# Optimization experiments

Hardware: AMD Instinct MI355X
Metric: run time of the kernel (lower is better)

The kernel has to match this reference:

```python
import jax, jax.numpy as jnp
import numpy as np
import math

B, T, C, NH = 4, 2048, 1024, 16
D = C // NH  # 64, rotary_dim == D

def _rope_tables():
    inv_freq = 1.0 / (10000.0 ** (np.arange(0, D, 2, dtype=np.float32) / D))
    t = np.arange(T, dtype=np.float32)
    freqs = np.outer(t, inv_freq)                 # [T, D/2]
    emb = np.concatenate([freqs, freqs], axis=-1)  # [T, D]
    return jnp.asarray(np.cos(emb))[None], jnp.asarray(np.sin(emb))[None]  # [1,T,D]

def setup_inputs() -> dict:
    key = jax.random.key(0)
    ks = jax.random.split(key, 3)
    x = jax.random.normal(ks[0], (B, T, C), dtype=jnp.float32)
    w_attn = jax.random.normal(ks[1], (3 * C, C), dtype=jnp.float32) * (1.0 / math.sqrt(C))
    b_attn = jnp.zeros((3 * C,), dtype=jnp.float32)
    w_proj = jax.random.normal(ks[2], (C, C), dtype=jnp.float32) * (1.0 / math.sqrt(C))
    b_proj = jnp.zeros((C,), dtype=jnp.float32)
    cos, sin = _rope_tables()
    return {"x": x, "w_attn": w_attn, "b_attn": b_attn,
            "w_proj": w_proj, "b_proj": b_proj, "cos": cos, "sin": sin}

def _rotate_half(u):
    u1, u2 = jnp.split(u, 2, axis=-1)
    return jnp.concatenate([-u2, u1], axis=-1)

def reference(x, w_attn, b_attn, w_proj, b_proj, cos, sin):
    Bx, Tx, Cx = x.shape
    nh, d = NH, Cx // NH
    # fused QKV projection (torch Linear: y = x @ W^T + b)
    qkv = x @ w_attn.T + b_attn                      # [B,T,3C]
    q, k, v = jnp.split(qkv, 3, axis=-1)
    q = q.reshape(Bx, Tx, nh, d).transpose(0, 2, 1, 3)  # [B,nh,T,d]
    k = k.reshape(Bx, Tx, nh, d).transpose(0, 2, 1, 3)
    v = v.reshape(Bx, Tx, nh, d).transpose(0, 2, 1, 3)
    # RoPE (rotary_dim == d, full head)
    c = cos[:, None, :, :]  # [1,1,T,d]
    s = sin[:, None, :, :]
    q = q * c + _rotate_half(q) * s
    k = k * c + _rotate_half(k) * s
    # naive causal attention
    scores = jnp.einsum("bhqd,bhkd->bhqk", q, k) / math.sqrt(d)
    causal = jnp.tril(jnp.ones((Tx, Tx), dtype=bool))
    scores = jnp.where(causal[None, None], scores, -jnp.inf)
    att = jax.nn.softmax(scores, axis=-1)
    y = jnp.einsum("bhqk,bhkd->bhqd", att, v)        # [B,nh,T,d]
    y = y.transpose(0, 2, 1, 3).reshape(Bx, Tx, Cx)
    return y @ w_proj.T + b_proj
```

## Files before the change

kernel.cpp:

```cpp
#include <hip/hip_runtime.h>

typedef __bf16 bf16_t;
typedef bf16_t bf16x8 __attribute__((ext_vector_type(8)));
typedef bf16_t bf16x4 __attribute__((ext_vector_type(4)));
typedef float f32x4 __attribute__((ext_vector_type(4)));

constexpr int BATCH = 4, SEQ = 2048, CH = 1024, NHEAD = 16, HD = 64;
constexpr int BM = 128, BN = 128, BKK = 64;

#define LGKM_FENCE() __asm__ __volatile__("s_waitcnt lgkmcnt(0)" ::: "memory")
#define VM_FENCE() __asm__ __volatile__("s_waitcnt vmcnt(0)" ::: "memory")

__device__ __forceinline__ void g2lds16(const bf16_t* g, bf16_t* l) {
  __builtin_amdgcn_global_load_lds((__attribute__((address_space(1))) void*)(g),
                                   (__attribute__((address_space(3))) void*)(l),
                                   16, 0, 0);
}

__device__ __forceinline__ f32x4 mfma16(bf16x8 a, bf16x8 b, f32x4 c) {
  return __builtin_amdgcn_mfma_f32_16x16x32_bf16(a, b, c, 0, 0, 0);
}

__global__ __launch_bounds__(256) void cvt3_kernel(const float4* __restrict__ x,
                                                   ushort4* __restrict__ dx,
                                                   const float4* __restrict__ wa,
                                                   ushort4* __restrict__ dwa,
                                                   const float4* __restrict__ wp,
                                                   ushort4* __restrict__ dwp) {
  int bid = blockIdx.x;
  const float4* s;
  ushort4* d;
  int i;
  if (bid < 8192) {
    s = x; d = dx; i = bid * 256 + threadIdx.x;
  } else if (bid < 11264) {
    s = wa; d = dwa; i = (bid - 8192) * 256 + threadIdx.x;
  } else {
    s = wp; d = dwp; i = (bid - 11264) * 256 + threadIdx.x;
  }
  float4 f = s[i];
  ushort4 o;
  o.x = __builtin_bit_cast(unsigned short, (bf16_t)f.x);
  o.y = __builtin_bit_cast(unsigned short, (bf16_t)f.y);
  o.z = __builtin_bit_cast(unsigned short, (bf16_t)f.z);
  o.w = __builtin_bit_cast(unsigned short, (bf16_t)f.w);
  d[i] = o;
}

__device__ __forceinline__ void gemm_mainloop(const bf16_t* __restrict__ A,
                                              const bf16_t* __restrict__ W, int Kdim,
                                              int m0, int n0,
                                              bf16_t* As, bf16_t* Bs,
                                              f32x4 acc[4][4]) {
  const int tid = threadIdx.x;
  const int lane = tid & 63;
  const int w = tid >> 6;
  const int quad = lane >> 4, l16 = lane & 15;
  const int wm = (w >> 1) << 6, wn = (w & 1) << 6;
  const int srow = tid >> 3;
  const int scol = ((tid & 7) ^ (srow & 7)) << 3;
  const int dcol = (tid & 7) << 3;
  const int key = l16 & 15 & 7;
  const bf16_t* ga[4];
  const bf16_t* gb[4];
  bf16_t *la[4], *lb[4];
#pragma unroll
  for (int p = 0; p < 4; p++) {
    int row = p * 32 + srow;
    ga[p] = A + (size_t)(m0 + row) * Kdim + scol;
    gb[p] = W + (size_t)(n0 + row) * Kdim + scol;
    la[p] = As + row * BKK + dcol;
    lb[p] = Bs + row * BKK + dcol;
  }
  for (int k0 = 0; k0 < Kdim; k0 += BKK) {
#pragma unroll
    for (int p = 0; p < 4; p++) g2lds16(ga[p] + k0, la[p]);
#pragma unroll
    for (int p = 0; p < 4; p++) g2lds16(gb[p] + k0, lb[p]);
    VM_FENCE();
    __syncthreads();
#pragma unroll
    for (int ki = 0; ki < 2; ki++) {
      bf16x8 av[4], bv[4];
#pragma unroll
      for (int i = 0; i < 4; i++)
        av[i] = *(const bf16x8*)&As[(wm + i * 16 + l16) * BKK +
                                    ((((ki << 2) | quad) ^ key) << 3)];
#pragma unroll
      for (int i = 0; i < 4; i++)
        bv[i] = *(const bf16x8*)&Bs[(wn + i * 16 + l16) * BKK +
                                    ((((ki << 2) | quad) ^ key) << 3)];
#pragma unroll
      for (int mi = 0; mi < 4; mi++)
#pragma unroll
        for (int ni = 0; ni < 4; ni++)
          acc[mi][ni] = mfma16(av[mi], bv[ni], acc[mi][ni]);
    }
    __syncthreads();
  }
}

constexpr float SCL = 0.125f * 1.44269504089f;

__global__ __launch_bounds__(256) void qkv_rope_kernel(
    const bf16_t* __restrict__ X, const bf16_t* __restrict__ Wa,
    const float* __restrict__ ba, const float* __restrict__ cosT,
    const float* __restrict__ sinT, bf16_t* __restrict__ Q,
    bf16_t* __restrict__ Ko, bf16_t* __restrict__ VT) {
  constexpr int TSTRIDE = 68;
  __shared__ __align__(16) char smem[4 * 64 * TSTRIDE * 2];
  bf16_t* As = (bf16_t*)smem;
  bf16_t* Bs = As + BM * BKK;

  f32x4 acc[4][4];
#pragma unroll
  for (int i = 0; i < 4; i++)
#pragma unroll
    for (int j = 0; j < 4; j++) acc[i][j] = (f32x4){0.f, 0.f, 0.f, 0.f};

  const int id = blockIdx.x;
  const int sid = ((id & 7) * 192) + (id >> 3);
  const int n0 = (sid % 24) * BN;
  const int m0 = (sid / 24) * BM;
  gemm_mainloop(X, Wa, CH, m0, n0, As, Bs, acc);

  const int tid = threadIdx.x, lane = tid & 63, w = tid >> 6;
  const int quad = lane >> 4, l16 = lane & 15;
  const int wm = (w >> 1) << 6, wn = (w & 1) << 6;
  const int nbase = n0 + wn;
  const int part = nbase >> 10;
  const int h = (nbase & 1023) >> 6;
  const int mbase = m0 + wm;
  const int bb = mbase >> 11;
  const size_t headbase = ((size_t)(bb * NHEAD + h)) * SEQ * HD;

  if (part < 2) {
    bf16_t* O = (part == 0) ? Q : Ko;
    const float post = (part == 0) ? SCL : 1.0f;
#pragma unroll
    for (int mi = 0; mi < 4; mi++)
#pragma unroll
      for (int r = 0; r < 4; r++) {
        int m = mbase + mi * 16 + quad * 4 + r;
        int t = m & (SEQ - 1);
        const float* cr = cosT + t * HD;
        const float* sr = sinT + t * HD;
        size_t rowo = headbase + (size_t)t * HD;
#pragma unroll
        for (int ni = 0; ni < 2; ni++) {
          int d0 = ni * 16 + l16, d1 = d0 + 32;
          float v0 = acc[mi][ni][r] + ba[nbase + d0];
          float v1 = acc[mi][ni + 2][r] + ba[nbase + d1];
          float r0 = (v0 * cr[d0] - v1 * sr[d0]) * post;
          float r1 = (v1 * cr[d1] + v0 * sr[d1]) * post;
          O[rowo + d0] = (bf16_t)r0;
          O[rowo + d1] = (bf16_t)r1;
        }
      }
  } else {
    bf16_t* tb = (bf16_t*)smem + w * 64 * TSTRIDE;
    int t0 = mbase & (SEQ - 1);
#pragma unroll
    for (int mi = 0; mi < 4; mi++)
#pragma unroll
      for (int ni = 0; ni < 4; ni++) {
        int d = ni * 16 + l16;
        float bias = ba[nbase + d];
#pragma unroll
        for (int r = 0; r < 4; r++) {
          float v = acc[mi][ni][r] + bias;
          tb[d * TSTRIDE + mi * 16 + quad * 4 + r] = (bf16_t)v;
        }
      }
    LGKM_FENCE();
    int half = lane >> 5, l5 = lane & 31;
    size_t vbase = ((size_t)(bb * NHEAD + h)) * HD * SEQ;
#pragma unroll
    for (int it = 0; it < 32; it++) {
      int d = it * 2 + half;
      unsigned int val = *(const unsigned int*)&tb[d * TSTRIDE + l5 * 2];
      *(unsigned int*)&VT[vbase + (size_t)d * SEQ + t0 + l5 * 2] = val;
    }
  }
}

__device__ __forceinline__ void sm_update(f32x4 (&s)[4], float& lr,
                                          bf16_t* Prow, int quad,
                                          int swz, bool domask, int lim) {
  if (domask) {
#pragma unroll
    for (int ni = 0; ni < 4; ni++)
#pragma unroll
      for (int r = 0; r < 4; r++)
        if (ni * 16 + r > lim) s[ni][r] = -1e30f;
  }
  float sum = 0.f;
#pragma unroll
  for (int ni = 0; ni < 4; ni++) {
    float p0 = __builtin_exp2f(s[ni][0]);
    float p1 = __builtin_exp2f(s[ni][1]);
    float p2 = __builtin_exp2f(s[ni][2]);
    float p3 = __builtin_exp2f(s[ni][3]);
    bf16x4 pk = {(bf16_t)p0, (bf16_t)p1, (bf16_t)p2, (bf16_t)p3};
    *(bf16x4*)&Prow[(((ni << 2) | quad) ^ (swz << 1)) << 2] = pk;
    sum += (p0 + p1) + (p2 + p3);
  }
  lr += sum;
}

__global__ __launch_bounds__(256) void flash_kernel(const bf16_t* __restrict__ Q,
                                                    const bf16_t* __restrict__ Kg,
                                                    const bf16_t* __restrict__ VT,
                                                    bf16_t* __restrict__ att) {
  __shared__ __align__(16) bf16_t Ks[2][64 * 64];
  __shared__ __align__(16) bf16_t Vs[2][64 * 64];
  __shared__ __align__(16) bf16_t Pt[4][16 * 64];
  const int tid = threadIdx.x, w = tid >> 6, lane = tid & 63;
  const int quad = lane >> 4, l16 = lane & 15;
  const int p = (int)blockIdx.x >> 6;
  const int bh = (int)blockIdx.x & 63;
  const bf16_t* Qp = Q + (size_t)bh * SEQ * HD;
  const bf16_t* Kb = Kg + (size_t)bh * SEQ * HD;
  const bf16_t* Vb = VT + (size_t)bh * HD * SEQ;
  const int grow = lane >> 3;
  const int gj8 = ((lane & 7) ^ grow) * 8;
  const int i0 = w * 2;
  const int sw = l16 & 7;
  const int swz = l16 >> 1;
  const int bloc = bh >> 4, hh = bh & 15;
  bf16_t* Pw = &Pt[w][l16 * 64];
  const int rs0 = (quad ^ swz) << 3;
  const int rs1 = ((4 + quad) ^ swz) << 3;

  auto stage = [&](int kcs, int b) {
#pragma unroll
    for (int ii = 0; ii < 2; ii++) {
      int i = i0 + ii;
      g2lds16(Kb + (size_t)(kcs + i * 8 + grow) * HD + gj8, &Ks[b][(i * 64 + lane) * 8]);
      g2lds16(Vb + (size_t)(i * 8 + grow) * SEQ + kcs + gj8, &Vs[b][(i * 64 + lane) * 8]);
    }
  };

  for (int sp = 0; sp < 2; ++sp) {
    const int j = sp ? p : 31 - p;
    const int m = j * 64 + w * 16;
    const int nch = j + 1;
    bf16x8 aq0 = *(const bf16x8*)&Qp[(size_t)(m + l16) * HD + quad * 8];
    bf16x8 aq1 = *(const bf16x8*)&Qp[(size_t)(m + l16) * HD + 32 + quad * 8];
    float lr = 0.f;
    f32x4 y[4];
#pragma unroll
    for (int ni = 0; ni < 4; ni++) y[ni] = (f32x4){0.f, 0.f, 0.f, 0.f};

    stage(0, 0);
    VM_FENCE();
    __syncthreads();

    for (int c = 0; c < nch; ++c) {
      const int kc = c * 64, buf = c & 1;
      if (c + 1 < nch) stage(kc + 64, buf ^ 1);
      f32x4 s[4];
#pragma unroll
      for (int ni = 0; ni < 4; ni++) {
        bf16x8 k0 = *(const bf16x8*)&Ks[buf][((ni * 16 + l16) * 8 + (quad ^ sw)) * 8];
        bf16x8 k1 = *(const bf16x8*)&Ks[buf][((ni * 16 + l16) * 8 + ((4 + quad) ^ sw)) * 8];
        f32x4 z = (f32x4){0.f, 0.f, 0.f, 0.f};
        s[ni] = mfma16(k1, aq1, mfma16(k0, aq0, z));
      }
      sm_update(s, lr, Pw, quad, swz, c == nch - 1, m + l16 - kc - quad * 4);
      LGKM_FENCE();
      bf16x8 p0 = *(const bf16x8*)&Pw[rs0];
      bf16x8 p1 = *(const bf16x8*)&Pw[rs1];
#pragma unroll
      for (int ni = 0; ni < 4; ni++) {
        bf16x8 v0 = *(const bf16x8*)&Vs[buf][((ni * 16 + l16) * 8 + (quad ^ sw)) * 8];
        bf16x8 v1 = *(const bf16x8*)&Vs[buf][((ni * 16 + l16) * 8 + ((4 + quad) ^ sw)) * 8];
        y[ni] = mfma16(v1, p1, mfma16(v0, p0, y[ni]));
      }
      VM_FENCE();
      __syncthreads();
    }

    lr += __shfl_xor(lr, 16);
    lr += __shfl_xor(lr, 32);
    float inv = 1.f / lr;
    size_t rb = ((size_t)bloc * SEQ + m + l16) * CH + hh * HD + quad * 4;
#pragma unroll
    for (int ni = 0; ni < 4; ni++) {
      bf16x4 o = {(bf16_t)(y[ni][0] * inv), (bf16_t)(y[ni][1] * inv),
                  (bf16_t)(y[ni][2] * inv), (bf16_t)(y[ni][3] * inv)};
      *(bf16x4*)&att[rb + ni * 16] = o;
    }
  }
}

__global__ __launch_bounds__(256) void proj_kernel(const bf16_t* __restrict__ A,
                                                   const bf16_t* __restrict__ Wp,
                                                   const float* __restrict__ bp,
                                                   float* __restrict__ out) {
  __shared__ __align__(16) bf16_t As[BM * BKK];
  __shared__ __align__(16) bf16_t Bs[BN * BKK];
  f32x4 acc[4][4];
#pragma unroll
  for (int i = 0; i < 4; i++)
#pragma unroll
    for (int j = 0; j < 4; j++) acc[i][j] = (f32x4){0.f, 0.f, 0.f, 0.f};
  const int id = blockIdx.x;
  const int sid = ((id & 7) * 64) + (id >> 3);
  const int n0 = (sid % 8) * BN;
  const int m0 = (sid / 8) * BM;
  gemm_mainloop(A, Wp, CH, m0, n0, As, Bs, acc);
  const int tid = threadIdx.x, lane = tid & 63, w = tid >> 6;
  const int quad = lane >> 4, l16 = lane & 15;
  const int wm = (w >> 1) << 6, wn = (w & 1) << 6;
  const int nbase = n0 + wn, mbase = m0 + wm;
#pragma unroll
  for (int mi = 0; mi < 4; mi++)
#pragma unroll
    for (int r = 0; r < 4; r++) {
      int m = mbase + mi * 16 + quad * 4 + r;
#pragma unroll
      for (int ni = 0; ni < 4; ni++) {
        int n = nbase + ni * 16 + l16;
        out[(size_t)m * CH + n] = acc[mi][ni][r] + bp[n];
      }
    }
}

extern "C" void kernel_launch(void* const* d_in, const int* in_sizes, int n_in,
                              void* d_out, int out_size, void* d_ws, size_t ws_size,
                              hipStream_t stream) {
  const float* x      = (const float*)d_in[0];
  const float* w_attn = (const float*)d_in[1];
  const float* b_attn = (const float*)d_in[2];
  const float* w_proj = (const float*)d_in[3];
  const float* b_proj = (const float*)d_in[4];
  const float* cosT   = (const float*)d_in[5];
  const float* sinT   = (const float*)d_in[6];
  float* out = (float*)d_out;

  bf16_t* xbf  = (bf16_t*)d_ws;
  bf16_t* wabf = xbf + (size_t)8192 * 1024;
  bf16_t* wpbf = wabf + (size_t)3072 * 1024;
  bf16_t* Qb   = wpbf + (size_t)1024 * 1024;
  bf16_t* Kb   = Qb + (size_t)8388608;
  bf16_t* VTb  = Kb + (size_t)8388608;
  bf16_t* attb = VTb + (size_t)8388608;

  cvt3_kernel<<<12288, 256, 0, stream>>>((const float4*)x, (ushort4*)xbf,
                                         (const float4*)w_attn, (ushort4*)wabf,
                                         (const float4*)w_proj, (ushort4*)wpbf);
  qkv_rope_kernel<<<dim3(1536), 256, 0, stream>>>(xbf, wabf, b_attn, cosT, sinT,
                                                  Qb, Kb, VTb);
  flash_kernel<<<dim3(1024), 256, 0, stream>>>(Qb, Kb, VTb, attb);
  proj_kernel<<<dim3(512), 256, 0, stream>>>(attb, wpbf, b_proj, out);
}
```

Before: 266.8 us.

## Widen flash blocks to 128 query rows and compute row sums via MFMA

The flash kernel now runs 8 waves per block covering 128 query rows, so each staged K/V chunk is shared by twice as many waves and half as many blocks are launched. Waves skip chunks that lie entirely beyond their causal limit, but they still join the barriers. The per-row softmax denominator is now accumulated with an extra MFMA against a ones vector, replacing the scalar sums and cross-lane shuffles. The cost is more idle waves on diagonal chunks and an extra MFMA pair per chunk, and fewer blocks may leave some compute units underused.

```diff
diff --git a/kernel.cpp b/kernel.cpp
--- a/kernel.cpp
+++ b/kernel.cpp
@@ -60,7 +60,7 @@
   const int srow = tid >> 3;
   const int scol = ((tid & 7) ^ (srow & 7)) << 3;
   const int dcol = (tid & 7) << 3;
-  const int key = l16 & 15 & 7;
+  const int key = l16 & 7;
   const bf16_t* ga[4];
   const bf16_t* gb[4];
   bf16_t *la[4], *lb[4];
@@ -184,8 +184,7 @@
   }
 }
 
-__device__ __forceinline__ void sm_update(f32x4 (&s)[4], float& lr,
-                                          bf16_t* Prow, int quad,
+__device__ __forceinline__ void sm_update(f32x4 (&s)[4], bf16_t* Prow, int quad,
                                           int swz, bool domask, int lim) {
   if (domask) {
 #pragma unroll
@@ -194,7 +193,6 @@
       for (int r = 0; r < 4; r++)
         if (ni * 16 + r > lim) s[ni][r] = -1e30f;
   }
-  float sum = 0.f;
 #pragma unroll
   for (int ni = 0; ni < 4; ni++) {
     float p0 = __builtin_exp2f(s[ni][0]);
@@ -203,18 +201,16 @@
     float p3 = __builtin_exp2f(s[ni][3]);
     bf16x4 pk = {(bf16_t)p0, (bf16_t)p1, (bf16_t)p2, (bf16_t)p3};
     *(bf16x4*)&Prow[(((ni << 2) | quad) ^ (swz << 1)) << 2] = pk;
-    sum += (p0 + p1) + (p2 + p3);
-  }
-  lr += sum;
-}
-
-__global__ __launch_bounds__(256) void flash_kernel(const bf16_t* __restrict__ Q,
-                                                    const bf16_t* __restrict__ Kg,
-                                                    const bf16_t* __restrict__ VT,
-                                                    bf16_t* __restrict__ att) {
+  }
+}
+
+__global__ __launch_bounds__(512, 4) void flash_kernel(const bf16_t* __restrict__ Q,
+                                                       const bf16_t* __restrict__ Kg,
+                                                       const bf16_t* __restrict__ VT,
+                                                       bf16_t* __restrict__ att) {
   __shared__ __align__(16) bf16_t Ks[2][64 * 64];
   __shared__ __align__(16) bf16_t Vs[2][64 * 64];
-  __shared__ __align__(16) bf16_t Pt[4][16 * 64];
+  __shared__ __align__(16) bf16_t Pt[8][16 * 64];
   const int tid = threadIdx.x, w = tid >> 6, lane = tid & 63;
   const int quad = lane >> 4, l16 = lane & 15;
   const int p = (int)blockIdx.x >> 6;
@@ -224,7 +220,6 @@
   const bf16_t* Vb = VT + (size_t)bh * HD * SEQ;
   const int grow = lane >> 3;
   const int gj8 = ((lane & 7) ^ grow) * 8;
-  const int i0 = w * 2;
   const int sw = l16 & 7;
   const int swz = l16 >> 1;
   const int bloc = bh >> 4, hh = bh & 15;
@@ -232,23 +227,22 @@
   const int rs0 = (quad ^ swz) << 3;
   const int rs1 = ((4 + quad) ^ swz) << 3;
 
+  const bf16x8 ones = {(bf16_t)1.f, (bf16_t)1.f, (bf16_t)1.f, (bf16_t)1.f,
+                       (bf16_t)1.f, (bf16_t)1.f, (bf16_t)1.f, (bf16_t)1.f};
+
   auto stage = [&](int kcs, int b) {
-#pragma unroll
-    for (int ii = 0; ii < 2; ii++) {
-      int i = i0 + ii;
-      g2lds16(Kb + (size_t)(kcs + i * 8 + grow) * HD + gj8, &Ks[b][(i * 64 + lane) * 8]);
-      g2lds16(Vb + (size_t)(i * 8 + grow) * SEQ + kcs + gj8, &Vs[b][(i * 64 + lane) * 8]);
-    }
+    g2lds16(Kb + (size_t)(kcs + w * 8 + grow) * HD + gj8, &Ks[b][(w * 64 + lane) * 8]);
+    g2lds16(Vb + (size_t)(w * 8 + grow) * SEQ + kcs + gj8, &Vs[b][(w * 64 + lane) * 8]);
   };
 
   for (int sp = 0; sp < 2; ++sp) {
-    const int j = sp ? p : 31 - p;
-    const int m = j * 64 + w * 16;
-    const int nch = j + 1;
+    const int jb = sp ? p : 15 - p;
+    const int m = jb * 128 + w * 16;
+    const int nch = 2 * jb + 2;
     bf16x8 aq0 = *(const bf16x8*)&Qp[(size_t)(m + l16) * HD + quad * 8];
     bf16x8 aq1 = *(const bf16x8*)&Qp[(size_t)(m + l16) * HD + 32 + quad * 8];
-    float lr = 0.f;
     f32x4 y[4];
+    f32x4 sum_acc = (f32x4){0.f, 0.f, 0.f, 0.f};
 #pragma unroll
     for (int ni = 0; ni < 4; ni++) y[ni] = (f32x4){0.f, 0.f, 0.f, 0.f};
 
@@ -259,31 +253,33 @@
     for (int c = 0; c < nch; ++c) {
       const int kc = c * 64, buf = c & 1;
       if (c + 1 < nch) stage(kc + 64, buf ^ 1);
-      f32x4 s[4];
-#pragma unroll
-      for (int ni = 0; ni < 4; ni++) {
-        bf16x8 k0 = *(const bf16x8*)&Ks[buf][((ni * 16 + l16) * 8 + (quad ^ sw)) * 8];
-        bf16x8 k1 = *(const bf16x8*)&Ks[buf][((ni * 16 + l16) * 8 + ((4 + quad) ^ sw)) * 8];
-        f32x4 z = (f32x4){0.f, 0.f, 0.f, 0.f};
-        s[ni] = mfma16(k1, aq1, mfma16(k0, aq0, z));
-      }
-      sm_update(s, lr, Pw, quad, swz, c == nch - 1, m + l16 - kc - quad * 4);
-      LGKM_FENCE();
-      bf16x8 p0 = *(const bf16x8*)&Pw[rs0];
-      bf16x8 p1 = *(const bf16x8*)&Pw[rs1];
-#pragma unroll
-      for (int ni = 0; ni < 4; ni++) {
-        bf16x8 v0 = *(const bf16x8*)&Vs[buf][((ni * 16 + l16) * 8 + (quad ^ sw)) * 8];
-        bf16x8 v1 = *(const bf16x8*)&Vs[buf][((ni * 16 + l16) * 8 + ((4 + quad) ^ sw)) * 8];
-        y[ni] = mfma16(v1, p1, mfma16(v0, p0, y[ni]));
+      const bool act = (kc <= m + 15);
+      if (act) {
+        f32x4 s[4];
+#pragma unroll
+        for (int ni = 0; ni < 4; ni++) {
+          bf16x8 k0 = *(const bf16x8*)&Ks[buf][((ni * 16 + l16) * 8 + (quad ^ sw)) * 8];
+          bf16x8 k1 = *(const bf16x8*)&Ks[buf][((ni * 16 + l16) * 8 + ((4 + quad) ^ sw)) * 8];
+          f32x4 z = (f32x4){0.f, 0.f, 0.f, 0.f};
+          s[ni] = mfma16(k1, aq1, mfma16(k0, aq0, z));
+        }
+        sm_update(s, Pw, quad, swz, kc + 63 > m, m + l16 - kc - quad * 4);
+        LGKM_FENCE();
+        bf16x8 p0 = *(const bf16x8*)&Pw[rs0];
+        bf16x8 p1 = *(const bf16x8*)&Pw[rs1];
+        sum_acc = mfma16(ones, p1, mfma16(ones, p0, sum_acc));
+#pragma unroll
+        for (int ni = 0; ni < 4; ni++) {
+          bf16x8 v0 = *(const bf16x8*)&Vs[buf][((ni * 16 + l16) * 8 + (quad ^ sw)) * 8];
+          bf16x8 v1 = *(const bf16x8*)&Vs[buf][((ni * 16 + l16) * 8 + ((4 + quad) ^ sw)) * 8];
+          y[ni] = mfma16(v1, p1, mfma16(v0, p0, y[ni]));
+        }
       }
       VM_FENCE();
       __syncthreads();
     }
 
-    lr += __shfl_xor(lr, 16);
-    lr += __shfl_xor(lr, 32);
-    float inv = 1.f / lr;
+    float inv = 1.f / sum_acc[0];
     size_t rb = ((size_t)bloc * SEQ + m + l16) * CH + hh * HD + quad * 4;
 #pragma unroll
     for (int ni = 0; ni < 4; ni++) {
@@ -352,6 +348,6 @@
                                          (const float4*)w_proj, (ushort4*)wpbf);
   qkv_rope_kernel<<<dim3(1536), 256, 0, stream>>>(xbf, wabf, b_attn, cosT, sinT,
                                                   Qb, Kb, VTb);
-  flash_kernel<<<dim3(1024), 256, 0, stream>>>(Qb, Kb, VTb, attb);
+  flash_kernel<<<dim3(512), 512, 0, stream>>>(Qb, Kb, VTb, attb);
   proj_kernel<<<dim3(512), 256, 0, stream>>>(attb, wpbf, b_proj, out);
 }
```

Measured after the change: 256.7 us. 1.04x faster.
